# Optimization experiments

Measured on AMD Instinct MI355X. Metric: run time of the kernel, lower is better.

The kernel has to match this reference:

```python
import jax, jax.numpy as jnp
import numpy as np

B, D, C, NS = 4, 64, 16, 4          # batch (clusters), spatial size, nPlanes (constant mode), num_strides
LEAK, EPS = 0.0, 1e-4               # leakiness_enc, SCN BatchNorm eps
N = 200_000                          # total points across clusters
DN = ('NCDHW', 'DHWIO', 'NCDHW')


def _conv(x, w, stride=1, pad='SAME'):
    return jax.lax.conv_general_dilated(x, w, (stride,) * 3, pad, dimension_numbers=DN)


def _bn_lrelu(x, m, gamma, beta):
    # BatchNormLeakyReLU over ACTIVE sites only (mask m is {0,1} float [B,1,d,d,d])
    n = jnp.maximum(jnp.sum(m), 1.0)
    mean = jnp.sum(x * m, axis=(0, 2, 3, 4)) / n
    xc = x - mean[None, :, None, None, None]
    var = jnp.sum((xc * xc) * m, axis=(0, 2, 3, 4)) / n
    xh = xc * jax.lax.rsqrt(var + EPS)[None, :, None, None, None]
    xh = xh * gamma[None, :, None, None, None] + beta[None, :, None, None, None]
    return jnp.where(xh > 0, xh, LEAK * xh) * m


def _down_mask(m):
    # SCN strided Convolution: output site active if any input site in its 2x2x2 window is active
    d = m.shape[2]
    return m.reshape(B, 1, d // 2, 2, d // 2, 2, d // 2, 2).max(axis=(3, 5, 7))


def setup_inputs() -> dict:
    key = jax.random.key(0)
    ks = jax.random.split(key, 12)
    coords = jax.random.randint(ks[0], (N, 3), 0, D).astype(jnp.float32)
    data = jnp.concatenate([coords, jnp.zeros((N, 2), jnp.float32)], axis=1)  # cols 3,4 overwritten in fwd
    clust_ids = jax.random.randint(ks[1], (N,), 0, B)
    s = 0.1
    return {
        'data': data,
        'clust_ids': clust_ids,
        'w_prep': jax.random.normal(ks[2], (3, 3, 3, 1, C)) * s,
        'enc_gamma': jnp.ones((NS - 1, C)),
        'enc_beta': jnp.zeros((NS - 1, C)),
        'enc_wsub': jax.random.normal(ks[3], (NS - 1, 3, 3, 3, C, C)) * s,
        'enc_wdown': jax.random.normal(ks[4], (NS - 1, 2, 2, 2, C, C)) * s,
        'dec_gamma': jnp.ones((NS - 1, C)),
        'dec_beta': jnp.zeros((NS - 1, C)),
        'dec_wup': jax.random.normal(ks[5], (NS - 1, 2, 2, 2, C, C)) * s,
        'dec_wsub3': jax.random.normal(ks[6], (NS - 1, 3, 3, 3, C, C)) * s,
        'dec_wsub4': jax.random.normal(ks[7], (NS - 1, 4, 4, 4, C, C)) * s,
        'w_out': jax.random.normal(ks[8], (3, 3, 3, C, 1)) * s,
    }


def reference(data, clust_ids, w_prep, enc_gamma, enc_beta, enc_wsub, enc_wdown,
              dec_gamma, dec_beta, dec_wup, dec_wsub3, dec_wsub4, w_out):
    # --- InputLayer (mode=3: sum duplicate coords); features are all ones ---
    ijk = data[:, :3].astype(jnp.int32)
    b = clust_ids.astype(jnp.int32)
    lin = ((b * D + ijk[:, 0]) * D + ijk[:, 1]) * D + ijk[:, 2]
    x = jnp.zeros((B * D * D * D,), jnp.float32).at[lin].add(1.0).reshape(B, 1, D, D, D)
    mask = (x > 0).astype(jnp.float32)  # active-site mask (submanifold semantics)

    # prepare: SubmanifoldConvolution(1 -> C, k=3, no bias)
    x = _conv(x, w_prep) * mask

    # encoder
    masks = []
    for i in range(NS - 1):
        masks.append(mask)
        x = _bn_lrelu(x, mask, enc_gamma[i], enc_beta[i])
        x = _conv(x, enc_wsub[i]) * mask                      # submanifold k=3
        x = _conv(x, enc_wdown[i], stride=2, pad='VALID')      # strided Convolution k=2 s=2
        mask = _down_mask(mask)
        x = x * mask
    # last encoder stage is an empty Sequential (identity)

    hidden = x.reshape(B, -1)  # SparseToDense + view: [B, C*(D/2^(NS-1))^3]

    # decoder
    for j in range(NS - 1):
        lvl = NS - 2 - j
        x = _bn_lrelu(x, mask, dec_gamma[j], dec_beta[j])
        mask = masks[lvl]  # FullConvolution restores encoder-level active set
        x = jax.lax.conv_transpose(x, dec_wup[j], (2, 2, 2), 'VALID', dimension_numbers=DN) * mask
        x = _conv(x, dec_wsub3[j]) * mask                      # submanifold k=3
        # SparsifyFCS: keep sites where feature channel 0 > 0 (applied twice; idempotent)
        mask = mask * (x[:, :1] > 0).astype(jnp.float32)
        x = x * mask
        x = _conv(x, dec_wsub4[j], pad=[(1, 2)] * 3) * mask    # submanifold k=4

    out = _conv(x, w_out) * mask                               # output: SubmanifoldConvolution(C -> 1, k=3)
    return hidden, out
```

## Files before the change

### kernel.cpp

```cpp
#include <hip/hip_runtime.h>

#define TPB 256
#define CTPB 512

__device__ __forceinline__ void fma4(float4& a, float s, const float4 b){
  a.x = fmaf(s,b.x,a.x); a.y = fmaf(s,b.y,a.y);
  a.z = fmaf(s,b.z,a.z); a.w = fmaf(s,b.w,a.w);
}

__device__ __forceinline__ int vox(int b,int z,int y,int x,int ld){
  return ((((((b<<ld)|z)<<ld)|y)<<ld)|x);
}

__device__ __forceinline__ float chan(const float4&a0,const float4&a1,const float4&a2,const float4&a3,int c){
  const float4& f = (c<4)?a0:((c<8)?a1:((c<12)?a2:a3));
  int r=c&3;
  return r==0?f.x:(r==1?f.y:(r==2?f.z:f.w));
}

__device__ __forceinline__ void append_list(bool a, int v, int* __restrict__ list, int* __restrict__ cnt){
  __shared__ int lcnt, lbase;
  __shared__ int woff[TPB/64];
  if(threadIdx.x==0) lcnt=0;
  __syncthreads();
  unsigned long long bl = __ballot(a);
  int lane = threadIdx.x & 63;
  int wv = threadIdx.x >> 6;
  if(lane==0){ int pop=__popcll(bl); woff[wv] = pop ? atomicAdd(&lcnt,pop) : 0; }
  __syncthreads();
  if(threadIdx.x==0 && lcnt) lbase = atomicAdd(cnt, lcnt);
  __syncthreads();
  if(a) list[lbase + woff[wv] + __popcll(bl & ((1ull<<lane)-1ull))] = v;
}

__device__ __forceinline__ void stats_reduce(const float4&a0,const float4&a1,const float4&a2,const float4&a3,
                                             float* red, float* __restrict__ gsums){
  int lane=threadIdx.x&63, wv=threadIdx.x>>6, nw=blockDim.x>>6;
  #pragma unroll
  for(int c=0;c<16;c++){
    float x = chan(a0,a1,a2,a3,c);
    float q = x*x;
    for(int o=32;o>0;o>>=1){ x+=__shfl_down(x,o,64); q+=__shfl_down(q,o,64); }
    if(lane==0){ red[wv*32+c]=x; red[wv*32+16+c]=q; }
  }
  __syncthreads();
  if(threadIdx.x<32){
    float t=0.f;
    for(int w=0;w<nw;w++) t+=red[w*32+threadIdx.x];
    atomicAdd(&gsums[threadIdx.x], t);
  }
}

__device__ __forceinline__ void stats_reduce4(const float4&a, float* red, float* __restrict__ gsums){
  int lane=threadIdx.x&63, wv=threadIdx.x>>6, nw=blockDim.x>>6;
  float sx[4]={a.x,a.y,a.z,a.w};
  float sq[4]={a.x*a.x,a.y*a.y,a.z*a.z,a.w*a.w};
  for(int o=32;o>=4;o>>=1){
    #pragma unroll
    for(int k=0;k<4;k++){ sx[k]+=__shfl_down(sx[k],o,64); sq[k]+=__shfl_down(sq[k],o,64); }
  }
  if(lane<4){
    #pragma unroll
    for(int k=0;k<4;k++){ red[wv*32+lane*4+k]=sx[k]; red[wv*32+16+lane*4+k]=sq[k]; }
  }
  __syncthreads();
  if(threadIdx.x<32){
    float t=0.f;
    for(int w=0;w<nw;w++) t+=red[w*32+threadIdx.x];
    atomicAdd(&gsums[threadIdx.x], t);
  }
}

__global__ __launch_bounds__(TPB) void k_scatter(const float* __restrict__ data, const int* __restrict__ cl,
                                                 int n, float* __restrict__ c0){
  int i = blockIdx.x*blockDim.x + threadIdx.x;
  if(i>=n) return;
  int z=(int)data[i*5+0], y=(int)data[i*5+1], x=(int)data[i*5+2];
  atomicAdd(&c0[vox(cl[i],z,y,x,6)], 1.0f);
}

__global__ __launch_bounds__(TPB) void k_cnt0(const float* __restrict__ c0, int n, int* __restrict__ bc){
  int i = blockIdx.x*TPB + threadIdx.x;
  bool a = (i<n) && (c0[i]>0.f);
  unsigned long long bl = __ballot(a);
  __shared__ int wcnt[TPB/64];
  int lane=threadIdx.x&63, wv=threadIdx.x>>6;
  if(lane==0) wcnt[wv]=__popcll(bl);
  __syncthreads();
  if(threadIdx.x==0) bc[blockIdx.x]=wcnt[0]+wcnt[1]+wcnt[2]+wcnt[3];
}

__global__ __launch_bounds__(1024) void k_scan0(int* __restrict__ bc, int nb, int* __restrict__ total){
  __shared__ int s[1024];
  int t=threadIdx.x, b4=t*4;
  int v0 = (b4+0<nb)?bc[b4+0]:0;
  int v1 = (b4+1<nb)?bc[b4+1]:0;
  int v2 = (b4+2<nb)?bc[b4+2]:0;
  int v3 = (b4+3<nb)?bc[b4+3]:0;
  int sum=v0+v1+v2+v3;
  s[t]=sum; __syncthreads();
  for(int o=1;o<1024;o<<=1){
    int x = (t>=o)? s[t-o] : 0;
    __syncthreads();
    s[t]+=x;
    __syncthreads();
  }
  int excl=s[t]-sum;
  if(b4+0<nb) bc[b4+0]=excl;
  if(b4+1<nb) bc[b4+1]=excl+v0;
  if(b4+2<nb) bc[b4+2]=excl+v0+v1;
  if(b4+3<nb) bc[b4+3]=excl+v0+v1+v2;
  if(t==1023) *total = s[1023];
}

__global__ __launch_bounds__(TPB) void k_emit0(const float* __restrict__ c0, int n,
                                               const int* __restrict__ bc, int* __restrict__ list){
  int i = blockIdx.x*TPB + threadIdx.x;
  bool a = (i<n) && (c0[i]>0.f);
  unsigned long long bl = __ballot(a);
  __shared__ int woff[TPB/64];
  __shared__ int wpre[TPB/64];
  int lane=threadIdx.x&63, wv=threadIdx.x>>6;
  if(lane==0) woff[wv]=__popcll(bl);
  __syncthreads();
  if(threadIdx.x==0){ int acc=0; for(int w=0;w<TPB/64;w++){ wpre[w]=acc; acc+=woff[w]; } }
  __syncthreads();
  if(a) list[bc[blockIdx.x] + wpre[wv] + __popcll(bl&((1ull<<lane)-1ull))] = i;
}

__global__ __launch_bounds__(TPB) void k_markparent_compact(const int* __restrict__ listF, const int* __restrict__ cntF,
        int ldf, int* __restrict__ g, int* __restrict__ listC, int* __restrict__ cntC){
  int i = blockIdx.x*TPB + threadIdx.x;
  bool first=false; int p=0;
  if(i < *cntF){
    int v=listF[i];
    int dm=(1<<ldf)-1;
    int x=v&dm, y=(v>>ldf)&dm, z=(v>>(2*ldf))&dm, b=v>>(3*ldf);
    p=vox(b,z>>1,y>>1,x>>1,ldf-1);
    first = (atomicExch(&g[p],1)==0);
  }
  append_list(first,p,listC,cntC);
}

__global__ __launch_bounds__(TPB) void k_sparsify_compact(float* __restrict__ X, float* __restrict__ Y,
        const int* __restrict__ listA, const int* __restrict__ cntA,
        int* __restrict__ listB, int* __restrict__ cntB, int* __restrict__ gmask){
  int i = blockIdx.x*TPB + threadIdx.x;
  bool keep=false; int v=0;
  if(i < *cntA){
    v = listA[i];
    keep = X[(size_t)v<<4] > 0.f;
    if(!keep){
      float4 zz = make_float4(0,0,0,0);
      float4* px=(float4*)(X+((size_t)v<<4)); px[0]=zz;px[1]=zz;px[2]=zz;px[3]=zz;
      float4* py=(float4*)(Y+((size_t)v<<4)); py[0]=zz;py[1]=zz;py[2]=zz;py[3]=zz;
      if(gmask) gmask[v]=0;
    }
  }
  append_list(keep,v,listB,cntB);
}

__global__ __launch_bounds__(TPB) void k_prep_l(const float* __restrict__ c0, const int* __restrict__ list,
          const int* __restrict__ cnt, const float* __restrict__ w, float* __restrict__ X,
          float* __restrict__ gsums){
  __shared__ float wl[432];
  __shared__ float red[(TPB/64)*32];
  for(int i=threadIdx.x;i<432;i+=TPB) wl[i]=w[i];
  __syncthreads();
  int i = blockIdx.x*TPB + threadIdx.x;
  bool act = i < *cnt;
  float4 a0=make_float4(0,0,0,0), a1=a0, a2=a0, a3=a0;
  if(act){
    int v=list[i];
    int x=v&63, y=(v>>6)&63, z=(v>>12)&63, b=v>>18;
    for(int dz=0;dz<3;dz++){ int zz=z+dz-1; if((unsigned)zz>=64u) continue;
      for(int dy=0;dy<3;dy++){ int yy=y+dy-1; if((unsigned)yy>=64u) continue;
        for(int dx=0;dx<3;dx++){ int xx=x+dx-1; if((unsigned)xx>=64u) continue;
          float av = c0[vox(b,zz,yy,xx,6)];
          if(av==0.f) continue;
          const float4* wv=(const float4*)&wl[((dz*3+dy)*3+dx)<<4];
          fma4(a0,av,wv[0]); fma4(a1,av,wv[1]); fma4(a2,av,wv[2]); fma4(a3,av,wv[3]);
        }
      }
    }
    float4* o=(float4*)(X+((size_t)v<<4));
    o[0]=a0;o[1]=a1;o[2]=a2;o[3]=a3;
  }
  stats_reduce(a0,a1,a2,a3,red,gsums);
}

__global__ __launch_bounds__(CTPB) void k_conv3_l(const float* __restrict__ Xin, const int* __restrict__ list,
      const int* __restrict__ cnt, const float* __restrict__ w, float* __restrict__ Xout, int ld){
  __shared__ float wl[6912];
  int nwork = *cnt;
  if((int)((blockIdx.x*CTPB)>>2) >= nwork) return;
  for(int i=threadIdx.x;i<6912;i+=CTPB) wl[i]=w[i];
  __syncthreads();
  int t = blockIdx.x*CTPB + threadIdx.x;
  int i = t>>2, sub = t&3;
  if(i >= nwork) return;
  int v = list[i];
  int d=1<<ld, dm=d-1;
  int x=v&dm, y=(v>>ld)&dm, z=(v>>(2*ld))&dm, b=v>>(3*ld);
  float4 acc=make_float4(0,0,0,0);
  for(int dz=0;dz<3;dz++){ int zz=z+dz-1; if((unsigned)zz>=(unsigned)d) continue;
    for(int dy=0;dy<3;dy++){ int yy=y+dy-1; if((unsigned)yy>=(unsigned)d) continue;
      const float* srow = Xin + ((size_t)vox(b,zz,yy,0,ld)<<4);
      const float* wrow = &wl[(((dz*3+dy)*3)<<8) + (sub<<2)];
      for(int dx=0;dx<3;dx++){ int xx=x+dx-1; if((unsigned)xx>=(unsigned)d) continue;
        const float4* sp=(const float4*)(srow + ((size_t)xx<<4));
        float s[16];
        *(float4*)&s[0]=sp[0]; *(float4*)&s[4]=sp[1]; *(float4*)&s[8]=sp[2]; *(float4*)&s[12]=sp[3];
        const float* wt = wrow + (dx<<8);
        #pragma unroll
        for(int ci=0;ci<16;ci++)
          fma4(acc, s[ci], *(const float4*)(wt + (ci<<4)));
      }
    }
  }
  ((float4*)(Xout + ((size_t)v<<4)))[sub] = acc;
}

__global__ __launch_bounds__(CTPB) void k_conv4_l(const float* __restrict__ Xin, const int* __restrict__ list,
      const int* __restrict__ cnt, const float* __restrict__ w, float* __restrict__ Xout, int ld,
      float* __restrict__ gsums){
  __shared__ float wl[8192];
  __shared__ float red[(CTPB/64)*32];
  int nwork = *cnt;
  if((int)((blockIdx.x*CTPB)>>2) >= nwork) return;
  int t = blockIdx.x*CTPB + threadIdx.x;
  int i = t>>2, sub = t&3;
  bool act = i < nwork;
  int v=0,x=0,y=0,z=0,b=0,d=1<<ld,dm=d-1;
  if(act){
    v = list[i];
    x=v&dm; y=(v>>ld)&dm; z=(v>>(2*ld))&dm; b=v>>(3*ld);
  }
  float4 acc=make_float4(0,0,0,0);
  for(int half=0;half<2;half++){
    __syncthreads();
    for(int k=threadIdx.x;k<8192;k+=CTPB) wl[k]=w[half*8192+k];
    __syncthreads();
    if(act){
      for(int dzl=0;dzl<2;dzl++){ int dz=half*2+dzl;
        int zz=z+dz-1; if((unsigned)zz>=(unsigned)d) continue;
        for(int dy=0;dy<4;dy++){ int yy=y+dy-1; if((unsigned)yy>=(unsigned)d) continue;
          const float* srow = Xin + ((size_t)vox(b,zz,yy,0,ld)<<4);
          const float* wrow = &wl[((dzl*4+dy)<<10) + (sub<<2)];
          for(int dx=0;dx<4;dx++){ int xx=x+dx-1; if((unsigned)xx>=(unsigned)d) continue;
            const float4* sp=(const float4*)(srow + ((size_t)xx<<4));
            float s[16];
            *(float4*)&s[0]=sp[0]; *(float4*)&s[4]=sp[1]; *(float4*)&s[8]=sp[2]; *(float4*)&s[12]=sp[3];
            const float* wt = wrow + (dx<<8);
            #pragma unroll
            for(int ci=0;ci<16;ci++)
              fma4(acc, s[ci], *(const float4*)(wt + (ci<<4)));
          }
        }
      }
    }
  }
  if(act) ((float4*)(Xout + ((size_t)v<<4)))[sub] = acc;
  __syncthreads();
  stats_reduce4(acc, red, gsums);
}

__global__ __launch_bounds__(TPB) void k_down_l(const float* __restrict__ Xin, const int* __restrict__ list,
      const int* __restrict__ cnt, const float* __restrict__ w, float* __restrict__ Xout, int ldc,
      float* __restrict__ gsums){
  __shared__ float wl[2048];
  __shared__ float red[(TPB/64)*32];
  int nwork = *cnt;
  for(int k=threadIdx.x;k<2048;k+=TPB) wl[k]=w[k];
  __syncthreads();
  int t = blockIdx.x*TPB + threadIdx.x;
  int i = t>>2, sub = t&3;
  bool act = i < nwork;
  float4 acc=make_float4(0,0,0,0);
  if(act){
    int v = list[i];
    int dm=(1<<ldc)-1, ldf=ldc+1;
    int x=v&dm, y=(v>>ldc)&dm, z=(v>>(2*ldc))&dm, b=v>>(3*ldc);
    for(int dz=0;dz<2;dz++) for(int dy=0;dy<2;dy++) for(int dx=0;dx<2;dx++){
      const float4* sp=(const float4*)(Xin + ((size_t)vox(b,2*z+dz,2*y+dy,2*x+dx,ldf)<<4));
      float s[16];
      *(float4*)&s[0]=sp[0]; *(float4*)&s[4]=sp[1]; *(float4*)&s[8]=sp[2]; *(float4*)&s[12]=sp[3];
      const float* wt=&wl[((((dz<<1)|dy)<<1 | dx)<<8) + (sub<<2)];
      #pragma unroll
      for(int ci=0;ci<16;ci++)
        fma4(acc, s[ci], *(const float4*)(wt+(ci<<4)));
    }
    ((float4*)(Xout+((size_t)v<<4)))[sub] = acc;
  }
  stats_reduce4(acc, red, gsums);
}

__global__ __launch_bounds__(TPB) void k_upbn_l(const float* __restrict__ Xc, const int* __restrict__ list,
      const int* __restrict__ cnt, const float* __restrict__ w,
      const float* __restrict__ sums, const int* __restrict__ bncnt,
      const float* __restrict__ g, const float* __restrict__ bta,
      const int* __restrict__ gmask, float* __restrict__ Xf, int ldf){
  __shared__ float wl[2048];
  __shared__ float sc[16], sh[16];
  for(int k=threadIdx.x;k<2048;k+=TPB) wl[k]=w[k];
  if(threadIdx.x<16){
    int c=threadIdx.x;
    float n=(float)(*bncnt); if(n<1.f) n=1.f;
    float mean=sums[c]/n;
    float var=sums[16+c]/n - mean*mean;
    float s=g[c]/sqrtf(var+1e-4f);
    sc[c]=s; sh[c]=fmaf(-mean,s,bta[c]);
  }
  __syncthreads();
  int i = blockIdx.x*TPB + threadIdx.x;
  if(i >= *cnt) return;
  int v = list[i];
  int dm=(1<<ldf)-1, ldc=ldf-1;
  int x=v&dm, y=(v>>ldf)&dm, z=(v>>(2*ldf))&dm, b=v>>(3*ldf);
  int p = vox(b,z>>1,y>>1,x>>1,ldc);
  float4 a0=make_float4(0,0,0,0), a1=a0, a2=a0, a3=a0;
  if(gmask[p]!=0){
    const float4* sp=(const float4*)(Xc + ((size_t)p<<4));
    float s[16];
    *(float4*)&s[0]=sp[0]; *(float4*)&s[4]=sp[1]; *(float4*)&s[8]=sp[2]; *(float4*)&s[12]=sp[3];
    #pragma unroll
    for(int ci=0;ci<16;ci++){ float xh=fmaf(s[ci],sc[ci],sh[ci]); s[ci]=xh>0.f?xh:0.f; }
    int tpar = ((((z&1)^1)<<1 | ((y&1)^1))<<1) | ((x&1)^1);
    const float* wt=&wl[tpar<<8];
    #pragma unroll
    for(int ci=0;ci<16;ci++){
      float av=s[ci];
      const float4* wv=(const float4*)(wt+(ci<<4));
      fma4(a0,av,wv[0]); fma4(a1,av,wv[1]); fma4(a2,av,wv[2]); fma4(a3,av,wv[3]);
    }
  }
  float4* o=(float4*)(Xf+((size_t)v<<4));
  o[0]=a0;o[1]=a1;o[2]=a2;o[3]=a3;
}

__global__ __launch_bounds__(TPB) void k_bnapply(float* __restrict__ X, const int* __restrict__ list,
        const int* __restrict__ cnt, const float* __restrict__ sums,
        const float* __restrict__ g, const float* __restrict__ bta){
  __shared__ float sc[16], sh[16];
  if(threadIdx.x<16){
    int c=threadIdx.x;
    float n=(float)(*cnt); if(n<1.f) n=1.f;
    float mean=sums[c]/n;
    float var=sums[16+c]/n - mean*mean;
    float s=g[c]/sqrtf(var+1e-4f);
    sc[c]=s; sh[c]=fmaf(-mean,s,bta[c]);
  }
  __syncthreads();
  int i = blockIdx.x*TPB + threadIdx.x;
  if(i>=*cnt) return;
  float* p = X + ((size_t)list[i]<<4);
  #pragma unroll
  for(int c=0;c<16;c++){
    float xh = fmaf(p[c], sc[c], sh[c]);
    p[c] = xh>0.f ? xh : 0.f;
  }
}

__global__ __launch_bounds__(TPB) void k_hidden(const float* __restrict__ X3, float* __restrict__ out){
  int i = blockIdx.x*TPB + threadIdx.x;
  if(i>=4*8192) return;
  int b=i>>13, r=i&8191, c=r>>9, s=r&511;
  out[i] = X3[(((size_t)((b<<9)|s))<<4)|c];
}

__global__ __launch_bounds__(TPB) void k_final_l(const float* __restrict__ Xin, const int* __restrict__ list,
      const int* __restrict__ cnt, const float* __restrict__ w, float* __restrict__ out){
  __shared__ float wl[432];
  for(int k=threadIdx.x;k<432;k+=TPB) wl[k]=w[k];
  __syncthreads();
  int i = blockIdx.x*TPB + threadIdx.x;
  if(i >= *cnt) return;
  int v = list[i];
  float acc=0.f;
  int x=v&63, y=(v>>6)&63, z=(v>>12)&63, b=v>>18;
  for(int dz=0;dz<3;dz++){ int zz=z+dz-1; if((unsigned)zz>=64u) continue;
    for(int dy=0;dy<3;dy++){ int yy=y+dy-1; if((unsigned)yy>=64u) continue;
      for(int dx=0;dx<3;dx++){ int xx=x+dx-1; if((unsigned)xx>=64u) continue;
        const float* sp = Xin + ((size_t)vox(b,zz,yy,xx,6)<<4);
        const float* wt = &wl[((dz*3+dy)*3+dx)<<4];
        #pragma unroll
        for(int ci=0;ci<16;ci++) acc = fmaf(sp[ci], wt[ci], acc);
      }
    }
  }
  out[v]=acc;
}

static inline int nb(int n){ return (n+TPB-1)/TPB; }
static inline int nbC(int n){ return (n+CTPB-1)/CTPB; }
static inline size_t rbytes(int ld){ return ((size_t)4<<(3*ld))*64; }

extern "C" void kernel_launch(void* const* d_in, const int* in_sizes, int n_in,
                              void* d_out, int out_size, void* d_ws, size_t ws_size,
                              hipStream_t stream){
  const float* data   = (const float*)d_in[0];
  const int*   cl     = (const int*)d_in[1];
  const float* w_prep = (const float*)d_in[2];
  const float* enc_g  = (const float*)d_in[3];
  const float* enc_b  = (const float*)d_in[4];
  const float* enc_ws = (const float*)d_in[5];
  const float* enc_wd = (const float*)d_in[6];
  const float* dec_g  = (const float*)d_in[7];
  const float* dec_b  = (const float*)d_in[8];
  const float* dec_wu = (const float*)d_in[9];
  const float* dec_w3 = (const float*)d_in[10];
  const float* dec_w4 = (const float*)d_in[11];
  const float* w_out  = (const float*)d_in[12];
  int N = in_sizes[0]/5;
  float* outp = (float*)d_out;

  const size_t FEAT_ROOMY = 38305792;
  const size_t FEAT_TIGHT = 33554432;
  const size_t TAILN      = 1048576 + 149504 + 224 + 16 + 4096 + 821248;
  bool roomy = ws_size >= (FEAT_ROOMY + TAILN)*sizeof(float);

  float* ws = (float*)d_ws;
  float *A[4]={0,0,0,0}, *B[4]={0,0,0,0}, *X=0, *Y=0;
  size_t featsz;
  if(roomy){
    A[0]=ws;            B[0]=A[0]+16777216;
    A[1]=B[0]+16777216; B[1]=A[1]+2097152;
    A[2]=B[1]+2097152;  B[2]=A[2]+262144;
    A[3]=B[2]+262144;
    featsz=FEAT_ROOMY;
  } else { X=ws; Y=X+16777216; featsz=FEAT_TIGHT; }
  float* c0 = ws + featsz;
  int* g1=(int*)(c0+1048576); int* g2=g1+131072; int* g3=g2+16384;
  float* sums=(float*)(g3+2048);
  int* counts=(int*)(sums+224);
  int* bc=counts+16;
  int* l0a=bc+4096; int* l0b=l0a+262144; int* l1a=l0b+262144; int* l1b=l1a+131072;
  int* l2a=l1b+131072; int* l2b=l2a+16384; int* l3=l2b+16384;
  int* la[4]={l0a,l1a,l2a,l3};
  int* lb[3]={l0b,l1b,l2b};
  int* g[4]={nullptr,g1,g2,g3};
  int b0 = N<262144?N:262144;
  int bounds[4]={b0,131072,16384,2048};

  hipMemsetAsync(ws, 0, featsz*sizeof(float), stream);
  hipMemsetAsync(c0, 0, (1048576+149504+224+16+4096)*sizeof(float), stream);

  k_scatter<<<nb(N),TPB,0,stream>>>(data, cl, N, c0);
  k_cnt0 <<<4096,TPB,0,stream>>>(c0, 1048576, bc);
  k_scan0<<<1,1024,0,stream>>>(bc, 4096, counts+0);
  k_emit0<<<4096,TPB,0,stream>>>(c0, 1048576, bc, l0a);

  if(roomy){
    k_prep_l<<<nb(b0),TPB,0,stream>>>(c0, l0a, counts+0, w_prep, A[0], sums);
    for(int i=0;i<3;i++){
      int ld=6-i;
      k_bnapply<<<nb(bounds[i]),TPB,0,stream>>>(A[i], la[i], counts+i, sums+32*i, enc_g+16*i, enc_b+16*i);
      k_conv3_l<<<nbC(4*bounds[i]),CTPB,0,stream>>>(A[i], la[i], counts+i, enc_ws+6912*i, B[i], ld);
      k_markparent_compact<<<nb(bounds[i]),TPB,0,stream>>>(la[i], counts+i, ld, g[i+1], la[i+1], counts+(i+1));
      k_down_l<<<nb(4*bounds[i+1]),TPB,0,stream>>>(B[i], la[i+1], counts+(i+1), enc_wd+2048*i, A[i+1], ld-1, sums+32*(i+1));
    }
    k_hidden<<<nb(32768),TPB,0,stream>>>(A[3], outp);
    for(int j=0;j<3;j++){
      int lvl=2-j, ldf=6-lvl;
      const int* bncnt = (j==0)? counts+3 : counts+4+(lvl+1);
      k_upbn_l<<<nb(bounds[lvl]),TPB,0,stream>>>(A[lvl+1], la[lvl], counts+lvl, dec_wu+2048*j,
            sums+32*(3+j), bncnt, dec_g+16*j, dec_b+16*j, g[lvl+1], A[lvl], ldf);
      k_conv3_l<<<nbC(4*bounds[lvl]),CTPB,0,stream>>>(A[lvl], la[lvl], counts+lvl, dec_w3+6912*j, B[lvl], ldf);
      k_sparsify_compact<<<nb(bounds[lvl]),TPB,0,stream>>>(B[lvl], A[lvl], la[lvl], counts+lvl, lb[lvl], counts+4+lvl, g[lvl]);
      float* ss = (j<2)? sums+32*(4+j) : sums+32*6;
      k_conv4_l<<<nbC(4*bounds[lvl]),CTPB,0,stream>>>(B[lvl], lb[lvl], counts+4+lvl, dec_w4+16384*j, A[lvl], ldf, ss);
    }
    hipMemsetAsync(outp+32768, 0, (size_t)1048576*sizeof(float), stream);
    k_final_l<<<nb(b0),TPB,0,stream>>>(A[0], lb[0], counts+4, w_out, outp+32768);
  } else {
    k_prep_l<<<nb(b0),TPB,0,stream>>>(c0, l0a, counts+0, w_prep, X, sums);
    float* cur=X; float* oth=Y; int ld=6;
    for(int i=0;i<3;i++){
      k_bnapply<<<nb(bounds[i]),TPB,0,stream>>>(cur, la[i], counts+i, sums+32*i, enc_g+16*i, enc_b+16*i);
      hipMemsetAsync(oth, 0, rbytes(ld), stream);
      k_conv3_l<<<nbC(4*bounds[i]),CTPB,0,stream>>>(cur, la[i], counts+i, enc_ws+6912*i, oth, ld);
      { float* t=cur; cur=oth; oth=t; }
      k_markparent_compact<<<nb(bounds[i]),TPB,0,stream>>>(la[i], counts+i, ld, g[i+1], la[i+1], counts+(i+1));
      hipMemsetAsync(oth, 0, rbytes(ld-1), stream);
      k_down_l<<<nb(4*bounds[i+1]),TPB,0,stream>>>(cur, la[i+1], counts+(i+1), enc_wd+2048*i, oth, ld-1, sums+32*(i+1));
      { float* t=cur; cur=oth; oth=t; }
      ld--;
    }
    k_hidden<<<nb(32768),TPB,0,stream>>>(cur, outp);
    for(int j=0;j<3;j++){
      int lvl=2-j, ldf=ld+1;
      const int* bncnt = (j==0)? counts+3 : counts+4+(lvl+1);
      hipMemsetAsync(oth, 0, rbytes(ldf), stream);
      k_upbn_l<<<nb(bounds[lvl]),TPB,0,stream>>>(cur, la[lvl], counts+lvl, dec_wu+2048*j,
            sums+32*(3+j), bncnt, dec_g+16*j, dec_b+16*j, g[lvl+1], oth, ldf);
      { float* t=cur; cur=oth; oth=t; }
      hipMemsetAsync(oth, 0, rbytes(ldf), stream);
      k_conv3_l<<<nbC(4*bounds[lvl]),CTPB,0,stream>>>(cur, la[lvl], counts+lvl, dec_w3+6912*j, oth, ldf);
      { float* t=cur; cur=oth; oth=t; }
      k_sparsify_compact<<<nb(bounds[lvl]),TPB,0,stream>>>(cur, oth, la[lvl], counts+lvl, lb[lvl], counts+4+lvl, g[lvl]);
      float* ss = (j<2)? sums+32*(4+j) : sums+32*6;
      k_conv4_l<<<nbC(4*bounds[lvl]),CTPB,0,stream>>>(cur, lb[lvl], counts+4+lvl, dec_w4+16384*j, oth, ldf, ss);
      { float* t=cur; cur=oth; oth=t; }
      ld=ldf;
    }
    hipMemsetAsync(outp+32768, 0, (size_t)1048576*sizeof(float), stream);
    k_final_l<<<nb(b0),TPB,0,stream>>>(cur, lb[0], counts+4, w_out, outp+32768);
  }
}
```

Baseline: 642.3 us.

## Gate sparse conv neighbor reads on activity grids and skip dense feature memset

Passes per-level activity grids to the conv3, conv4, downsample and final kernels so they load and accumulate only neighbours that are active, instead of reading zeros from inactive voxels. Because inactive sites are never read, the roomy path drops the large memset that zeroed the whole feature workspace and clears only the small bottleneck buffer. The trade is an extra int load per neighbour and branches that can diverge. Correctness relies on the grids exactly matching the sites written at every level, including the sparsified decoder set and the reuse of the c0 occupancy buffer at level 0.

```diff
diff --git a/kernel.cpp b/kernel.cpp
--- a/kernel.cpp
+++ b/kernel.cpp
@@ -190,7 +190,8 @@
 }
 
 __global__ __launch_bounds__(CTPB) void k_conv3_l(const float* __restrict__ Xin, const int* __restrict__ list,
-      const int* __restrict__ cnt, const float* __restrict__ w, float* __restrict__ Xout, int ld){
+      const int* __restrict__ cnt, const float* __restrict__ w, const int* __restrict__ actg,
+      float* __restrict__ Xout, int ld){
   __shared__ float wl[6912];
   int nwork = *cnt;
   if((int)((blockIdx.x*CTPB)>>2) >= nwork) return;
@@ -205,9 +206,17 @@
   float4 acc=make_float4(0,0,0,0);
   for(int dz=0;dz<3;dz++){ int zz=z+dz-1; if((unsigned)zz>=(unsigned)d) continue;
     for(int dy=0;dy<3;dy++){ int yy=y+dy-1; if((unsigned)yy>=(unsigned)d) continue;
-      const float* srow = Xin + ((size_t)vox(b,zz,yy,0,ld)<<4);
+      int rb = vox(b,zz,yy,0,ld);
+      const float* srow = Xin + ((size_t)rb<<4);
+      const int* arow = actg + rb;
+      int m[3];
+      #pragma unroll
+      for(int dx=0;dx<3;dx++){ int xx=x+dx-1; m[dx] = ((unsigned)xx<(unsigned)d) ? arow[xx] : 0; }
       const float* wrow = &wl[(((dz*3+dy)*3)<<8) + (sub<<2)];
-      for(int dx=0;dx<3;dx++){ int xx=x+dx-1; if((unsigned)xx>=(unsigned)d) continue;
+      #pragma unroll
+      for(int dx=0;dx<3;dx++){
+        if(!m[dx]) continue;
+        int xx=x+dx-1;
         const float4* sp=(const float4*)(srow + ((size_t)xx<<4));
         float s[16];
         *(float4*)&s[0]=sp[0]; *(float4*)&s[4]=sp[1]; *(float4*)&s[8]=sp[2]; *(float4*)&s[12]=sp[3];
@@ -222,8 +231,8 @@
 }
 
 __global__ __launch_bounds__(CTPB) void k_conv4_l(const float* __restrict__ Xin, const int* __restrict__ list,
-      const int* __restrict__ cnt, const float* __restrict__ w, float* __restrict__ Xout, int ld,
-      float* __restrict__ gsums){
+      const int* __restrict__ cnt, const float* __restrict__ w, const int* __restrict__ actg,
+      float* __restrict__ Xout, int ld, float* __restrict__ gsums){
   __shared__ float wl[8192];
   __shared__ float red[(CTPB/64)*32];
   int nwork = *cnt;
@@ -245,9 +254,17 @@
       for(int dzl=0;dzl<2;dzl++){ int dz=half*2+dzl;
         int zz=z+dz-1; if((unsigned)zz>=(unsigned)d) continue;
         for(int dy=0;dy<4;dy++){ int yy=y+dy-1; if((unsigned)yy>=(unsigned)d) continue;
-          const float* srow = Xin + ((size_t)vox(b,zz,yy,0,ld)<<4);
+          int rb = vox(b,zz,yy,0,ld);
+          const float* srow = Xin + ((size_t)rb<<4);
+          const int* arow = actg + rb;
+          int m[4];
+          #pragma unroll
+          for(int dx=0;dx<4;dx++){ int xx=x+dx-1; m[dx] = ((unsigned)xx<(unsigned)d) ? arow[xx] : 0; }
           const float* wrow = &wl[((dzl*4+dy)<<10) + (sub<<2)];
-          for(int dx=0;dx<4;dx++){ int xx=x+dx-1; if((unsigned)xx>=(unsigned)d) continue;
+          #pragma unroll
+          for(int dx=0;dx<4;dx++){
+            if(!m[dx]) continue;
+            int xx=x+dx-1;
             const float4* sp=(const float4*)(srow + ((size_t)xx<<4));
             float s[16];
             *(float4*)&s[0]=sp[0]; *(float4*)&s[4]=sp[1]; *(float4*)&s[8]=sp[2]; *(float4*)&s[12]=sp[3];
@@ -266,8 +283,8 @@
 }
 
 __global__ __launch_bounds__(TPB) void k_down_l(const float* __restrict__ Xin, const int* __restrict__ list,
-      const int* __restrict__ cnt, const float* __restrict__ w, float* __restrict__ Xout, int ldc,
-      float* __restrict__ gsums){
+      const int* __restrict__ cnt, const float* __restrict__ w, const int* __restrict__ actf,
+      float* __restrict__ Xout, int ldc, float* __restrict__ gsums){
   __shared__ float wl[2048];
   __shared__ float red[(TPB/64)*32];
   int nwork = *cnt;
@@ -282,7 +299,9 @@
     int dm=(1<<ldc)-1, ldf=ldc+1;
     int x=v&dm, y=(v>>ldc)&dm, z=(v>>(2*ldc))&dm, b=v>>(3*ldc);
     for(int dz=0;dz<2;dz++) for(int dy=0;dy<2;dy++) for(int dx=0;dx<2;dx++){
-      const float4* sp=(const float4*)(Xin + ((size_t)vox(b,2*z+dz,2*y+dy,2*x+dx,ldf)<<4));
+      int fi = vox(b,2*z+dz,2*y+dy,2*x+dx,ldf);
+      if(!actf[fi]) continue;
+      const float4* sp=(const float4*)(Xin + ((size_t)fi<<4));
       float s[16];
       *(float4*)&s[0]=sp[0]; *(float4*)&s[4]=sp[1]; *(float4*)&s[8]=sp[2]; *(float4*)&s[12]=sp[3];
       const float* wt=&wl[((((dz<<1)|dy)<<1 | dx)<<8) + (sub<<2)];
@@ -369,7 +388,8 @@
 }
 
 __global__ __launch_bounds__(TPB) void k_final_l(const float* __restrict__ Xin, const int* __restrict__ list,
-      const int* __restrict__ cnt, const float* __restrict__ w, float* __restrict__ out){
+      const int* __restrict__ cnt, const float* __restrict__ w, const int* __restrict__ actg,
+      float* __restrict__ out){
   __shared__ float wl[432];
   for(int k=threadIdx.x;k<432;k+=TPB) wl[k]=w[k];
   __syncthreads();
@@ -380,8 +400,16 @@
   int x=v&63, y=(v>>6)&63, z=(v>>12)&63, b=v>>18;
   for(int dz=0;dz<3;dz++){ int zz=z+dz-1; if((unsigned)zz>=64u) continue;
     for(int dy=0;dy<3;dy++){ int yy=y+dy-1; if((unsigned)yy>=64u) continue;
-      for(int dx=0;dx<3;dx++){ int xx=x+dx-1; if((unsigned)xx>=64u) continue;
-        const float* sp = Xin + ((size_t)vox(b,zz,yy,xx,6)<<4);
+      int rb = vox(b,zz,yy,0,6);
+      const int* arow = actg + rb;
+      int m[3];
+      #pragma unroll
+      for(int dx=0;dx<3;dx++){ int xx=x+dx-1; m[dx] = ((unsigned)xx<64u) ? arow[xx] : 0; }
+      #pragma unroll
+      for(int dx=0;dx<3;dx++){
+        if(!m[dx]) continue;
+        int xx=x+dx-1;
+        const float* sp = Xin + ((size_t)(rb+xx)<<4);
         const float* wt = &wl[((dz*3+dy)*3+dx)<<4];
         #pragma unroll
         for(int ci=0;ci<16;ci++) acc = fmaf(sp[ci], wt[ci], acc);
@@ -439,10 +467,15 @@
   int* la[4]={l0a,l1a,l2a,l3};
   int* lb[3]={l0b,l1b,l2b};
   int* g[4]={nullptr,g1,g2,g3};
+  int* actF[4]={(int*)c0, g1, g2, g3};
   int b0 = N<262144?N:262144;
   int bounds[4]={b0,131072,16384,2048};
 
-  hipMemsetAsync(ws, 0, featsz*sizeof(float), stream);
+  if(roomy){
+    hipMemsetAsync(A[3], 0, 32768*sizeof(float), stream);
+  } else {
+    hipMemsetAsync(ws, 0, featsz*sizeof(float), stream);
+  }
   hipMemsetAsync(c0, 0, (1048576+149504+224+16+4096)*sizeof(float), stream);
 
   k_scatter<<<nb(N),TPB,0,stream>>>(data, cl, N, c0);
@@ -455,9 +488,9 @@
     for(int i=0;i<3;i++){
       int ld=6-i;
       k_bnapply<<<nb(bounds[i]),TPB,0,stream>>>(A[i], la[i], counts+i, sums+32*i, enc_g+16*i, enc_b+16*i);
-      k_conv3_l<<<nbC(4*bounds[i]),CTPB,0,stream>>>(A[i], la[i], counts+i, enc_ws+6912*i, B[i], ld);
+      k_conv3_l<<<nbC(4*bounds[i]),CTPB,0,stream>>>(A[i], la[i], counts+i, enc_ws+6912*i, actF[i], B[i], ld);
       k_markparent_compact<<<nb(bounds[i]),TPB,0,stream>>>(la[i], counts+i, ld, g[i+1], la[i+1], counts+(i+1));
-      k_down_l<<<nb(4*bounds[i+1]),TPB,0,stream>>>(B[i], la[i+1], counts+(i+1), enc_wd+2048*i, A[i+1], ld-1, sums+32*(i+1));
+      k_down_l<<<nb(4*bounds[i+1]),TPB,0,stream>>>(B[i], la[i+1], counts+(i+1), enc_wd+2048*i, actF[i], A[i+1], ld-1, sums+32*(i+1));
     }
     k_hidden<<<nb(32768),TPB,0,stream>>>(A[3], outp);
     for(int j=0;j<3;j++){
@@ -465,24 +498,24 @@
       const int* bncnt = (j==0)? counts+3 : counts+4+(lvl+1);
       k_upbn_l<<<nb(bounds[lvl]),TPB,0,stream>>>(A[lvl+1], la[lvl], counts+lvl, dec_wu+2048*j,
             sums+32*(3+j), bncnt, dec_g+16*j, dec_b+16*j, g[lvl+1], A[lvl], ldf);
-      k_conv3_l<<<nbC(4*bounds[lvl]),CTPB,0,stream>>>(A[lvl], la[lvl], counts+lvl, dec_w3+6912*j, B[lvl], ldf);
+      k_conv3_l<<<nbC(4*bounds[lvl]),CTPB,0,stream>>>(A[lvl], la[lvl], counts+lvl, dec_w3+6912*j, actF[lvl], B[lvl], ldf);
       k_sparsify_compact<<<nb(bounds[lvl]),TPB,0,stream>>>(B[lvl], A[lvl], la[lvl], counts+lvl, lb[lvl], counts+4+lvl, g[lvl]);
       float* ss = (j<2)? sums+32*(4+j) : sums+32*6;
-      k_conv4_l<<<nbC(4*bounds[lvl]),CTPB,0,stream>>>(B[lvl], lb[lvl], counts+4+lvl, dec_w4+16384*j, A[lvl], ldf, ss);
+      k_conv4_l<<<nbC(4*bounds[lvl]),CTPB,0,stream>>>(B[lvl], lb[lvl], counts+4+lvl, dec_w4+16384*j, actF[lvl], A[lvl], ldf, ss);
     }
     hipMemsetAsync(outp+32768, 0, (size_t)1048576*sizeof(float), stream);
-    k_final_l<<<nb(b0),TPB,0,stream>>>(A[0], lb[0], counts+4, w_out, outp+32768);
+    k_final_l<<<nb(b0),TPB,0,stream>>>(A[0], lb[0], counts+4, w_out, actF[0], outp+32768);
   } else {
     k_prep_l<<<nb(b0),TPB,0,stream>>>(c0, l0a, counts+0, w_prep, X, sums);
     float* cur=X; float* oth=Y; int ld=6;
     for(int i=0;i<3;i++){
       k_bnapply<<<nb(bounds[i]),TPB,0,stream>>>(cur, la[i], counts+i, sums+32*i, enc_g+16*i, enc_b+16*i);
       hipMemsetAsync(oth, 0, rbytes(ld), stream);
-      k_conv3_l<<<nbC(4*bounds[i]),CTPB,0,stream>>>(cur, la[i], counts+i, enc_ws+6912*i, oth, ld);
+      k_conv3_l<<<nbC(4*bounds[i]),CTPB,0,stream>>>(cur, la[i], counts+i, enc_ws+6912*i, actF[i], oth, ld);
       { float* t=cur; cur=oth; oth=t; }
       k_markparent_compact<<<nb(bounds[i]),TPB,0,stream>>>(la[i], counts+i, ld, g[i+1], la[i+1], counts+(i+1));
       hipMemsetAsync(oth, 0, rbytes(ld-1), stream);
-      k_down_l<<<nb(4*bounds[i+1]),TPB,0,stream>>>(cur, la[i+1], counts+(i+1), enc_wd+2048*i, oth, ld-1, sums+32*(i+1));
+      k_down_l<<<nb(4*bounds[i+1]),TPB,0,stream>>>(cur, la[i+1], counts+(i+1), enc_wd+2048*i, actF[i], oth, ld-1, sums+32*(i+1));
       { float* t=cur; cur=oth; oth=t; }
       ld--;
     }
@@ -495,15 +528,15 @@
             sums+32*(3+j), bncnt, dec_g+16*j, dec_b+16*j, g[lvl+1], oth, ldf);
       { float* t=cur; cur=oth; oth=t; }
       hipMemsetAsync(oth, 0, rbytes(ldf), stream);
-      k_conv3_l<<<nbC(4*bounds[lvl]),CTPB,0,stream>>>(cur, la[lvl], counts+lvl, dec_w3+6912*j, oth, ldf);
+      k_conv3_l<<<nbC(4*bounds[lvl]),CTPB,0,stream>>>(cur, la[lvl], counts+lvl, dec_w3+6912*j, actF[lvl], oth, ldf);
       { float* t=cur; cur=oth; oth=t; }
       k_sparsify_compact<<<nb(bounds[lvl]),TPB,0,stream>>>(cur, oth, la[lvl], counts+lvl, lb[lvl], counts+4+lvl, g[lvl]);
       float* ss = (j<2)? sums+32*(4+j) : sums+32*6;
-      k_conv4_l<<<nbC(4*bounds[lvl]),CTPB,0,stream>>>(cur, lb[lvl], counts+4+lvl, dec_w4+16384*j, oth, ldf, ss);
+      k_conv4_l<<<nbC(4*bounds[lvl]),CTPB,0,stream>>>(cur, lb[lvl], counts+4+lvl, dec_w4+16384*j, actF[lvl], oth, ldf, ss);
       { float* t=cur; cur=oth; oth=t; }
       ld=ldf;
     }
     hipMemsetAsync(outp+32768, 0, (size_t)1048576*sizeof(float), stream);
-    k_final_l<<<nb(b0),TPB,0,stream>>>(cur, lb[0], counts+4, w_out, outp+32768);
-  }
-}
+    k_final_l<<<nb(b0),TPB,0,stream>>>(cur, lb[0], counts+4, w_out, actF[0], outp+32768);
+  }
+}
```

After: 726.5 us. 13.1% more time.
